# Kernel optimization log

Hardware: AMD Instinct MI355X
Metric: run time of the kernel (lower is better)

The kernel has to match this reference:

```python
import jax, jax.numpy as jnp
import numpy as np

EMB = 1024
HEADS = 16
HEAD_DIM = EMB // HEADS
DFF = 4 * EMB
EPS = 1e-5


def gelu_tanh(x):
    c = jnp.sqrt(jnp.asarray(2.0 / jnp.pi, dtype=x.dtype))
    return 0.5 * x * (1.0 + jnp.tanh(c * (x + 0.044715 * x ** 3)))


def layernorm(x, scale, shift):
    mean = jnp.mean(x, axis=-1, keepdims=True)
    var = jnp.mean((x - mean) ** 2, axis=-1, keepdims=True)
    return scale * ((x - mean) / jnp.sqrt(var + EPS)) + shift


def setup_inputs() -> dict:
    key = jax.random.key(0)
    ks = jax.random.split(key, 12)
    s = 0.02
    return {
        "x": jax.random.normal(ks[0], (2, 2048, EMB), dtype=jnp.float32),
        "Wq": jax.random.normal(ks[1], (EMB, EMB), dtype=jnp.float32) * s,
        "Wk": jax.random.normal(ks[2], (EMB, EMB), dtype=jnp.float32) * s,
        "Wv": jax.random.normal(ks[3], (EMB, EMB), dtype=jnp.float32) * s,
        "Wo": jax.random.normal(ks[4], (EMB, EMB), dtype=jnp.float32) * s,
        "bo": jnp.zeros((EMB,), dtype=jnp.float32),
        "W1": jax.random.normal(ks[5], (EMB, DFF), dtype=jnp.float32) * s,
        "b1": jnp.zeros((DFF,), dtype=jnp.float32),
        "W2": jax.random.normal(ks[6], (DFF, EMB), dtype=jnp.float32) * s,
        "b2": jnp.zeros((EMB,), dtype=jnp.float32),
        "g1": jnp.ones((EMB,), dtype=jnp.float32),
        "s1": jnp.zeros((EMB,), dtype=jnp.float32),
        "g2": jnp.ones((EMB,), dtype=jnp.float32),
        "s2": jnp.zeros((EMB,), dtype=jnp.float32),
    }


def reference(x, Wq, Wk, Wv, Wo, bo, W1, b1, W2, b2, g1, s1, g2, s2):
    B, S, E = x.shape
    # attention sub-block (pre-norm, residual)
    h = layernorm(x, g1, s1)
    Q = (h @ Wq).reshape(B, S, HEADS, HEAD_DIM)
    K = (h @ Wk).reshape(B, S, HEADS, HEAD_DIM)
    V = (h @ Wv).reshape(B, S, HEADS, HEAD_DIM)
    # scores: [B, H, S, S]
    scores = jnp.einsum("bqhd,bkhd->bhqk", Q, K)
    causal = jnp.tril(jnp.ones((S, S), dtype=bool))
    scores = jnp.where(causal, scores, -jnp.inf)
    attn = jax.nn.softmax(scores / np.sqrt(HEAD_DIM), axis=-1)
    ctx = jnp.einsum("bhqk,bkhd->bqhd", attn, V).reshape(B, S, E)
    x = x + (ctx @ Wo + bo)
    # FFN sub-block
    h = layernorm(x, g2, s2)
    h = gelu_tanh(h @ W1 + b1) @ W2 + b2
    return x + h
```

## Files before the change

### kernel.cpp

```cpp
#include <hip/hip_runtime.h>
#include <hip/hip_bf16.h>

typedef __attribute__((ext_vector_type(8))) short short8;
typedef __attribute__((ext_vector_type(4))) float f32x4;

#define EMB   1024
#define DFF   4096
#define S_LEN 2048
#define NB    2
#define MTOT  (NB * S_LEN)
#define HEADS 16
#define HDIM  64
#define QKVN  3072
#define BK    32

__device__ __forceinline__ float bf2f(unsigned short u) {
  return __uint_as_float(((unsigned int)u) << 16);
}
__device__ __forceinline__ unsigned short f2bf(float f) {
  unsigned int x = __float_as_uint(f);
  unsigned int r = (x + 0x7fffu + ((x >> 16) & 1u)) >> 16;
  return (unsigned short)r;
}
__device__ __forceinline__ unsigned int cvtpk(float a, float b) {
  unsigned int r;
  asm("v_cvt_pk_bf16_f32 %0, %1, %2" : "=v"(r) : "v"(a), "v"(b));
  return r;
}

__device__ __forceinline__ void gl_lds16(const unsigned short* g, unsigned short* l) {
  __builtin_amdgcn_global_load_lds(
      (const __attribute__((address_space(1))) unsigned int*)g,
      (__attribute__((address_space(3))) unsigned int*)l, 16, 0, 0);
}

__global__ __launch_bounds__(256) void transpose_to_bf16(
    const float* __restrict__ W, unsigned short* __restrict__ Wt, int K, int N)
{
  __shared__ float t[32][33];
  const int n0 = blockIdx.x * 32, k0 = blockIdx.y * 32;
  const int tx = threadIdx.x, ty = threadIdx.y;
#pragma unroll
  for (int i = 0; i < 4; ++i) {
    int r = ty + i * 8;
    t[r][tx] = W[(size_t)(k0 + r) * N + n0 + tx];
  }
  __syncthreads();
#pragma unroll
  for (int i = 0; i < 4; ++i) {
    int r = ty + i * 8;
    Wt[(size_t)(n0 + r) * K + k0 + tx] = f2bf(t[tx][r]);
  }
}

__global__ __launch_bounds__(256) void transpose_v(
    const unsigned short* __restrict__ qkv, unsigned short* __restrict__ Vt)
{
  __shared__ unsigned short t[32][33];
  const int s0 = blockIdx.x * 32, d0 = blockIdx.y * 32, bh = blockIdx.z;
  const int b = bh >> 4, h = bh & 15;
  const int tx = threadIdx.x, ty = threadIdx.y;
#pragma unroll
  for (int i = 0; i < 4; ++i) {
    int r = ty + i * 8;
    t[r][tx] = qkv[((size_t)(b * S_LEN + s0 + r)) * QKVN + 2048 + h * HDIM + d0 + tx];
  }
  __syncthreads();
#pragma unroll
  for (int i = 0; i < 4; ++i) {
    int r = ty + i * 8;
    Vt[((size_t)bh * HDIM + d0 + r) * S_LEN + s0 + tx] = t[tx][r];
  }
}

__global__ __launch_bounds__(256) void ln_kernel(
    const float* __restrict__ X, const float* __restrict__ g,
    const float* __restrict__ sh, unsigned short* __restrict__ H)
{
  const int row = blockIdx.x, t = threadIdx.x;
  const float* xr = X + (size_t)row * EMB;
  float4 v = *(const float4*)(xr + t * 4);
  float s  = v.x + v.y + v.z + v.w;
  float ss = v.x * v.x + v.y * v.y + v.z * v.z + v.w * v.w;
#pragma unroll
  for (int off = 32; off > 0; off >>= 1) {
    s  += __shfl_xor(s, off);
    ss += __shfl_xor(ss, off);
  }
  __shared__ float rs[4], rss[4];
  const int wid = t >> 6;
  if ((t & 63) == 0) { rs[wid] = s; rss[wid] = ss; }
  __syncthreads();
  s  = rs[0] + rs[1] + rs[2] + rs[3];
  ss = rss[0] + rss[1] + rss[2] + rss[3];
  const float mean = s * (1.f / EMB);
  const float var  = ss * (1.f / EMB) - mean * mean;
  const float rstd = rsqrtf(var + 1e-5f);
  float4 gv = *(const float4*)(g + t * 4);
  float4 sv = *(const float4*)(sh + t * 4);
  ushort4 o;
  o.x = f2bf((v.x - mean) * rstd * gv.x + sv.x);
  o.y = f2bf((v.y - mean) * rstd * gv.y + sv.y);
  o.z = f2bf((v.z - mean) * rstd * gv.z + sv.z);
  o.w = f2bf((v.w - mean) * rstd * gv.w + sv.w);
  *(ushort4*)(H + (size_t)row * EMB + t * 4) = o;
}

__device__ __forceinline__ float gelu_tanh_f(float v) {
  float u = v + 0.044715f * v * v * v;
  float t = tanhf(0.7978845608028654f * u);
  return 0.5f * v * (1.0f + t);
}

template <int MODE, int BN>
__global__ __launch_bounds__(256, 2) void gemm_gl(
    const unsigned short* __restrict__ A, const unsigned short* __restrict__ Bt,
    int M, int N, int Kloop, int Kld,
    const float* __restrict__ bias, const float* __restrict__ resf,
    float* __restrict__ outf, unsigned short* __restrict__ outb)
{
  constexpr int NFRAG = BN / 32;
  __shared__ unsigned short As[2][128 * BK];
  __shared__ unsigned short Bs[2][BN * BK];

  const int tid = threadIdx.x;
  const int lane = tid & 63, wid = tid >> 6;
  const int m0 = blockIdx.y * 128, n0 = blockIdx.x * BN;
  const int wr = wid >> 1, wc = wid & 1;
  const int l16 = lane & 15, kg = lane >> 4;

  const int sr  = lane >> 2;
  const int scs = (((lane & 3) ^ ((lane >> 3) & 3))) * 8;
  const int xr = (l16 >> 1) & 3;

  const unsigned short* Abase = A + (size_t)m0 * Kld;
  const unsigned short* Bbase = Bt + (size_t)n0 * Kld;

  f32x4 acc[4][NFRAG];
#pragma unroll
  for (int i = 0; i < 4; ++i)
#pragma unroll
    for (int j = 0; j < NFRAG; ++j) acc[i][j] = (f32x4){0.f, 0.f, 0.f, 0.f};

  const int nt = Kloop / BK;

#define STAGE(buf, t)                                                          \
  do {                                                                         \
    const int k0_ = (t) * BK;                                                  \
    _Pragma("unroll")                                                          \
    for (int i_ = 0; i_ < 2; ++i_) {                                           \
      const int chunk_ = wid * 2 + i_;                                         \
      gl_lds16(Abase + (size_t)(chunk_ * 16 + sr) * Kld + k0_ + scs,           \
               &As[buf][0] + chunk_ * 512);                                    \
    }                                                                          \
    _Pragma("unroll")                                                          \
    for (int i_ = 0; i_ < BN / 64; ++i_) {                                     \
      const int chunk_ = wid * (BN / 64) + i_;                                 \
      gl_lds16(Bbase + (size_t)(chunk_ * 16 + sr) * Kld + k0_ + scs,           \
               &Bs[buf][0] + chunk_ * 512);                                    \
    }                                                                          \
  } while (0)

  STAGE(0, 0);
  __syncthreads();
  int cur = 0;
  for (int t = 0; t < nt; ++t) {
    if (t + 1 < nt) STAGE(cur ^ 1, t + 1);
    short8 af[4], bfr[NFRAG];
#pragma unroll
    for (int i = 0; i < 4; ++i)
      af[i] = *(const short8*)(&As[cur][(wr * 64 + i * 16 + l16) * BK + (kg ^ xr) * 8]);
#pragma unroll
    for (int j = 0; j < NFRAG; ++j)
      bfr[j] = *(const short8*)(&Bs[cur][(wc * (BN / 2) + j * 16 + l16) * BK + (kg ^ xr) * 8]);
#pragma unroll
    for (int i = 0; i < 4; ++i)
#pragma unroll
      for (int j = 0; j < NFRAG; ++j)
        acc[i][j] = __builtin_amdgcn_mfma_f32_16x16x32_bf16(af[i], bfr[j], acc[i][j], 0, 0, 0);
    __syncthreads();
    cur ^= 1;
  }
#undef STAGE

#pragma unroll
  for (int i = 0; i < 4; ++i) {
#pragma unroll
    for (int j = 0; j < NFRAG; ++j) {
      const int c = n0 + wc * (BN / 2) + j * 16 + l16;
#pragma unroll
      for (int r = 0; r < 4; ++r) {
        const int row = m0 + wr * 64 + i * 16 + kg * 4 + r;
        const size_t idx = (size_t)row * N + c;
        float v = acc[i][j][r];
        if constexpr (MODE == 0) {
          outb[idx] = f2bf(c < 1024 ? v * 0.18033688011112042f : v);
        } else if constexpr (MODE == 1) {
          outf[idx] = v + bias[c] + resf[idx];
        } else if constexpr (MODE == 2) {
          outb[idx] = f2bf(gelu_tanh_f(v + bias[c]));
        } else if constexpr (MODE == 3) {
          outf[idx] = v + bias[c] + resf[idx];
        } else if constexpr (MODE == 4) {
          outb[idx] = f2bf(v);
        } else {
          outf[idx] = v + bias[c] + resf[idx] + bf2f(outb[idx]);
        }
      }
    }
  }
}

__global__ __launch_bounds__(256) void attn_mfma(
    const unsigned short* __restrict__ qkv, const unsigned short* __restrict__ Vt,
    unsigned short* __restrict__ ctx)
{
  __shared__ unsigned short Ks[64][64];
  __shared__ unsigned short Vs[64][64];
  __shared__ unsigned short Ps[4][2][16][64];

  const int tid  = threadIdx.x;
  const int lane = tid & 63, wv = tid >> 6;
  const int l16  = lane & 15, kg = lane >> 4;
  const int bh   = blockIdx.y;
  const int b    = bh >> 4, h = bh & 15;
  const int qtg0 = (int)blockIdx.x;
  const int qtg1 = 31 - (int)blockIdx.x;

  const size_t qbase  = ((size_t)b * S_LEN) * QKVN + h * HDIM;
  const size_t kbase  = qbase + 1024;
  const size_t vtbase = ((size_t)bh * HDIM) * S_LEN;
  const size_t cbase  = ((size_t)b * S_LEN) * EMB + h * HDIM;

  short8 qf[2][2];
#pragma unroll
  for (int g = 0; g < 2; ++g) {
    const int qt = g ? qtg1 : qtg0;
    const unsigned short* qrow =
        qkv + qbase + (size_t)(qt * 64 + wv * 16 + l16) * QKVN;
    qf[g][0] = *(const short8*)(qrow + kg * 8);
    qf[g][1] = *(const short8*)(qrow + 32 + kg * 8);
  }

  f32x4 o[2][4];
#pragma unroll
  for (int g = 0; g < 2; ++g)
#pragma unroll
    for (int dt = 0; dt < 4; ++dt) o[g][dt] = (f32x4){0.f, 0.f, 0.f, 0.f};
  float m[2] = {-1e30f, -1e30f}, l[2] = {0.f, 0.f};

  const int srow = tid >> 2;
  const int c0   = tid & 3;
  const int sx   = srow & 7;
  const int col0 = ((2 * c0)     ^ sx) * 8;
  const int col1 = ((2 * c0 + 1) ^ sx) * 8;
  const int rx   = l16 & 7;
  const int ntiles = qtg1 + 1;

  const unsigned short* ksrc = qkv + kbase + (size_t)srow * QKVN + c0 * 16;
  const unsigned short* vsrc = Vt + vtbase + (size_t)srow * S_LEN + c0 * 16;
  short8 k0 = *(const short8*)(ksrc);
  short8 k1 = *(const short8*)(ksrc + 8);
  short8 v0 = *(const short8*)(vsrc);
  short8 v1 = *(const short8*)(vsrc + 8);

  for (int kt = 0; kt < ntiles; ++kt) {
    __syncthreads();
    *(short8*)(&Ks[srow][col0]) = k0;
    *(short8*)(&Ks[srow][col1]) = k1;
    *(short8*)(&Vs[srow][col0]) = v0;
    *(short8*)(&Vs[srow][col1]) = v1;
    __syncthreads();

    if (kt + 1 < ntiles) {
      const unsigned short* kn =
          qkv + kbase + (size_t)((kt + 1) * 64 + srow) * QKVN + c0 * 16;
      const unsigned short* vn =
          Vt + vtbase + (size_t)srow * S_LEN + (kt + 1) * 64 + c0 * 16;
      k0 = *(const short8*)(kn);
      k1 = *(const short8*)(kn + 8);
      v0 = *(const short8*)(vn);
      v1 = *(const short8*)(vn + 8);
    }

    const bool act0 = (kt <= qtg0);

    short8 kf0[4], kf1[4];
#pragma unroll
    for (int j = 0; j < 4; ++j) {
      kf0[j] = *(const short8*)(&Ks[j * 16 + l16][(kg ^ rx) * 8]);
      kf1[j] = *(const short8*)(&Ks[j * 16 + l16][((kg + 4) ^ rx) * 8]);
    }

    float fac[2] = {1.f, 1.f};
#pragma unroll
    for (int g = 0; g < 2; ++g) {
      if (g == 0 && !act0) continue;
      const int qt = g ? qtg1 : qtg0;

      f32x4 sa[4];
#pragma unroll
      for (int j = 0; j < 4; ++j) {
        sa[j] = (f32x4){0.f, 0.f, 0.f, 0.f};
        sa[j] = __builtin_amdgcn_mfma_f32_16x16x32_bf16(kf0[j], qf[g][0], sa[j], 0, 0, 0);
        sa[j] = __builtin_amdgcn_mfma_f32_16x16x32_bf16(kf1[j], qf[g][1], sa[j], 0, 0, 0);
      }

      if (kt == qt) {
        const int qloc = wv * 16 + l16;
#pragma unroll
        for (int j = 0; j < 4; ++j)
#pragma unroll
          for (int r = 0; r < 4; ++r)
            if (j * 16 + kg * 4 + r > qloc) sa[j][r] = -1e30f;
      }

      float m0j = fmaxf(fmaxf(sa[0][0], sa[0][1]), fmaxf(sa[0][2], sa[0][3]));
      float m1j = fmaxf(fmaxf(sa[1][0], sa[1][1]), fmaxf(sa[1][2], sa[1][3]));
      float m2j = fmaxf(fmaxf(sa[2][0], sa[2][1]), fmaxf(sa[2][2], sa[2][3]));
      float m3j = fmaxf(fmaxf(sa[3][0], sa[3][1]), fmaxf(sa[3][2], sa[3][3]));
      float mx = fmaxf(fmaxf(m0j, m1j), fmaxf(m2j, m3j));
      mx = fmaxf(mx, __shfl_xor(mx, 16));
      mx = fmaxf(mx, __shfl_xor(mx, 32));
      const float mn = fmaxf(m[g], mx);
      fac[g] = exp2f(m[g] - mn);
      m[g] = mn;
      float ps = 0.f;
#pragma unroll
      for (int j = 0; j < 4; ++j) {
        float p0 = exp2f(sa[j][0] - mn);
        float p1 = exp2f(sa[j][1] - mn);
        float p2 = exp2f(sa[j][2] - mn);
        float p3 = exp2f(sa[j][3] - mn);
        sa[j][0] = p0; sa[j][1] = p1; sa[j][2] = p2; sa[j][3] = p3;
        ps += (p0 + p1) + (p2 + p3);
      }
      ps += __shfl_xor(ps, 16);
      ps += __shfl_xor(ps, 32);
      l[g] = l[g] * fac[g] + ps;

#pragma unroll
      for (int j = 0; j < 4; ++j) {
        uint2 pw;
        pw.x = cvtpk(sa[j][0], sa[j][1]);
        pw.y = cvtpk(sa[j][2], sa[j][3]);
        *(uint2*)(&Ps[wv][g][l16][((2 * j + (kg >> 1)) ^ rx) * 8 + (kg & 1) * 4]) = pw;
      }
    }

#pragma unroll
    for (int g = 0; g < 2; ++g) {
      if (g == 0 && !act0) continue;
#pragma unroll
      for (int dt = 0; dt < 4; ++dt)
#pragma unroll
        for (int r = 0; r < 4; ++r) o[g][dt][r] *= fac[g];
    }

    short8 pf[2][2];
#pragma unroll
    for (int g = 0; g < 2; ++g) {
      if (g == 0 && !act0) continue;
      pf[g][0] = *(const short8*)(&Ps[wv][g][l16][(kg ^ rx) * 8]);
      pf[g][1] = *(const short8*)(&Ps[wv][g][l16][((kg + 4) ^ rx) * 8]);
    }
#pragma unroll
    for (int dt = 0; dt < 4; ++dt) {
      short8 vf0 = *(const short8*)(&Vs[dt * 16 + l16][(kg ^ rx) * 8]);
      short8 vf1 = *(const short8*)(&Vs[dt * 16 + l16][((kg + 4) ^ rx) * 8]);
#pragma unroll
      for (int g = 0; g < 2; ++g) {
        if (g == 0 && !act0) continue;
        o[g][dt] = __builtin_amdgcn_mfma_f32_16x16x32_bf16(vf0, pf[g][0], o[g][dt], 0, 0, 0);
        o[g][dt] = __builtin_amdgcn_mfma_f32_16x16x32_bf16(vf1, pf[g][1], o[g][dt], 0, 0, 0);
      }
    }
  }

#pragma unroll
  for (int g = 0; g < 2; ++g) {
    const int qt = g ? qtg1 : qtg0;
    const float inv = 1.0f / l[g];
    const int qrow = qt * 64 + wv * 16 + l16;
#pragma unroll
    for (int dt = 0; dt < 4; ++dt) {
      uint2 cw;
      cw.x = cvtpk(o[g][dt][0] * inv, o[g][dt][1] * inv);
      cw.y = cvtpk(o[g][dt][2] * inv, o[g][dt][3] * inv);
      *(uint2*)(&ctx[cbase + (size_t)qrow * EMB + dt * 16 + kg * 4]) = cw;
    }
  }
}

extern "C" void kernel_launch(void* const* d_in, const int* in_sizes, int n_in,
                              void* d_out, int out_size, void* d_ws, size_t ws_size,
                              hipStream_t stream)
{
  const float* x  = (const float*)d_in[0];
  const float* Wq = (const float*)d_in[1];
  const float* Wk = (const float*)d_in[2];
  const float* Wv = (const float*)d_in[3];
  const float* Wo = (const float*)d_in[4];
  const float* bo = (const float*)d_in[5];
  const float* W1 = (const float*)d_in[6];
  const float* b1 = (const float*)d_in[7];
  const float* W2 = (const float*)d_in[8];
  const float* b2 = (const float*)d_in[9];
  const float* g1 = (const float*)d_in[10];
  const float* s1 = (const float*)d_in[11];
  const float* g2 = (const float*)d_in[12];
  const float* s2 = (const float*)d_in[13];

  float* out = (float*)d_out;
  char* ws = (char*)d_ws;
  const size_t MB = 1024 * 1024;
  unsigned short* wtQ  = (unsigned short*)(ws + 0 * MB);
  unsigned short* wtK  = (unsigned short*)(ws + 2 * MB);
  unsigned short* wtV  = (unsigned short*)(ws + 4 * MB);
  unsigned short* wtO  = (unsigned short*)(ws + 6 * MB);
  unsigned short* wtW1 = (unsigned short*)(ws + 8 * MB);
  unsigned short* wtW2 = (unsigned short*)(ws + 16 * MB);
  unsigned short* h    = (unsigned short*)(ws + 24 * MB);
  unsigned short* qkv  = (unsigned short*)(ws + 32 * MB);
  unsigned short* Vt   = (unsigned short*)(ws + 56 * MB);
  unsigned short* ctxb = h;
  unsigned short* h2   = h;
  unsigned short* pbuf = h;
  unsigned short* gbuf = qkv;

  dim3 tb(32, 8);
  transpose_to_bf16<<<dim3(32, 32),  tb, 0, stream>>>(Wq, wtQ, 1024, 1024);
  transpose_to_bf16<<<dim3(32, 32),  tb, 0, stream>>>(Wk, wtK, 1024, 1024);
  transpose_to_bf16<<<dim3(32, 32),  tb, 0, stream>>>(Wv, wtV, 1024, 1024);
  transpose_to_bf16<<<dim3(32, 32),  tb, 0, stream>>>(Wo, wtO, 1024, 1024);
  transpose_to_bf16<<<dim3(128, 32), tb, 0, stream>>>(W1, wtW1, 1024, 4096);
  transpose_to_bf16<<<dim3(32, 128), tb, 0, stream>>>(W2, wtW2, 4096, 1024);

  ln_kernel<<<MTOT, 256, 0, stream>>>(x, g1, s1, h);

  gemm_gl<0, 128><<<dim3(24, 32), 256, 0, stream>>>(
      h, wtQ, MTOT, QKVN, 1024, 1024, nullptr, nullptr, nullptr, qkv);

  transpose_v<<<dim3(64, 2, 32), tb, 0, stream>>>(qkv, Vt);

  attn_mfma<<<dim3(16, 32), 256, 0, stream>>>(qkv, Vt, ctxb);

  gemm_gl<1, 64><<<dim3(16, 32), 256, 0, stream>>>(
      ctxb, wtO, MTOT, 1024, 1024, 1024, bo, x, out, nullptr);

  ln_kernel<<<MTOT, 256, 0, stream>>>(out, g2, s2, h2);

  gemm_gl<2, 128><<<dim3(32, 32), 256, 0, stream>>>(
      h2, wtW1, MTOT, DFF, 1024, 1024, b1, nullptr, nullptr, gbuf);

  gemm_gl<4, 64><<<dim3(16, 32), 256, 0, stream>>>(
      gbuf + 2048, wtW2 + 2048, MTOT, 1024, 2048, DFF, nullptr, nullptr, nullptr, pbuf);
  gemm_gl<5, 64><<<dim3(16, 32), 256, 0, stream>>>(
      gbuf, wtW2, MTOT, 1024, 2048, DFF, b2, out, out, pbuf);
}
```

Baseline: 287.4 us.

## Fuse weight transposes, XCD-swizzle GEMM/attention grids, add lazy softmax rescale and setprio

```diff
diff --git a/kernel.cpp b/kernel.cpp
--- a/kernel.cpp
+++ b/kernel.cpp
@@ -34,11 +34,28 @@
       (__attribute__((address_space(3))) unsigned int*)l, 16, 0, 0);
 }
 
-__global__ __launch_bounds__(256) void transpose_to_bf16(
-    const float* __restrict__ W, unsigned short* __restrict__ Wt, int K, int N)
+__global__ __launch_bounds__(256) void fused_transpose(
+    const float* __restrict__ Wq, const float* __restrict__ Wk,
+    const float* __restrict__ Wv, const float* __restrict__ Wo,
+    const float* __restrict__ W1, const float* __restrict__ W2,
+    unsigned short* __restrict__ wtQ, unsigned short* __restrict__ wtK,
+    unsigned short* __restrict__ wtV, unsigned short* __restrict__ wtO,
+    unsigned short* __restrict__ wtW1, unsigned short* __restrict__ wtW2)
 {
   __shared__ float t[32][33];
-  const int n0 = blockIdx.x * 32, k0 = blockIdx.y * 32;
+  const int bid = (int)blockIdx.x;
+  const float* W; unsigned short* Wt; int K, N, local;
+  if (bid < 4096) {
+    const int sel = bid >> 10; local = bid & 1023; K = 1024; N = 1024;
+    W  = sel == 0 ? Wq  : sel == 1 ? Wk  : sel == 2 ? Wv  : Wo;
+    Wt = sel == 0 ? wtQ : sel == 1 ? wtK : sel == 2 ? wtV : wtO;
+  } else if (bid < 8192) {
+    local = bid - 4096; K = 1024; N = 4096; W = W1; Wt = wtW1;
+  } else {
+    local = bid - 8192; K = 4096; N = 1024; W = W2; Wt = wtW2;
+  }
+  const int nbx = N >> 5;
+  const int n0 = (local % nbx) * 32, k0 = (local / nbx) * 32;
   const int tx = threadIdx.x, ty = threadIdx.y;
 #pragma unroll
   for (int i = 0; i < 4; ++i) {
@@ -115,7 +132,7 @@
 template <int MODE, int BN>
 __global__ __launch_bounds__(256, 2) void gemm_gl(
     const unsigned short* __restrict__ A, const unsigned short* __restrict__ Bt,
-    int M, int N, int Kloop, int Kld,
+    int M, int N, int Kloop, int Kld, int nbx,
     const float* __restrict__ bias, const float* __restrict__ resf,
     float* __restrict__ outf, unsigned short* __restrict__ outb)
 {
@@ -125,7 +142,13 @@
 
   const int tid = threadIdx.x;
   const int lane = tid & 63, wid = tid >> 6;
-  const int m0 = blockIdx.y * 128, n0 = blockIdx.x * BN;
+  const int nwg = (int)gridDim.x;
+  const int cpx = nwg >> 3;
+  const int bid = (int)blockIdx.x;
+  const int swz = (bid & 7) * cpx + (bid >> 3);
+  const int by = swz / nbx;
+  const int bx = swz - by * nbx;
+  const int m0 = by * 128, n0 = bx * BN;
   const int wr = wid >> 1, wc = wid & 1;
   const int l16 = lane & 15, kg = lane >> 4;
 
@@ -199,8 +222,6 @@
           outf[idx] = v + bias[c] + resf[idx];
         } else if constexpr (MODE == 2) {
           outb[idx] = f2bf(gelu_tanh_f(v + bias[c]));
-        } else if constexpr (MODE == 3) {
-          outf[idx] = v + bias[c] + resf[idx];
         } else if constexpr (MODE == 4) {
           outb[idx] = f2bf(v);
         } else {
@@ -222,10 +243,13 @@
   const int tid  = threadIdx.x;
   const int lane = tid & 63, wv = tid >> 6;
   const int l16  = lane & 15, kg = lane >> 4;
-  const int bh   = blockIdx.y;
+  const int bid  = (int)blockIdx.x;
+  const int swz  = (bid & 7) * 64 + (bid >> 3);
+  const int pair = swz & 15;
+  const int bh   = swz >> 4;
   const int b    = bh >> 4, h = bh & 15;
-  const int qtg0 = (int)blockIdx.x;
-  const int qtg1 = 31 - (int)blockIdx.x;
+  const int qtg0 = pair;
+  const int qtg1 = 31 - pair;
 
   const size_t qbase  = ((size_t)b * S_LEN) * QKVN + h * HDIM;
   const size_t kbase  = qbase + 1024;
@@ -293,18 +317,21 @@
     }
 
     float fac[2] = {1.f, 1.f};
+    bool resc[2] = {false, false};
 #pragma unroll
     for (int g = 0; g < 2; ++g) {
       if (g == 0 && !act0) continue;
       const int qt = g ? qtg1 : qtg0;
 
       f32x4 sa[4];
+      __builtin_amdgcn_s_setprio(1);
 #pragma unroll
       for (int j = 0; j < 4; ++j) {
         sa[j] = (f32x4){0.f, 0.f, 0.f, 0.f};
         sa[j] = __builtin_amdgcn_mfma_f32_16x16x32_bf16(kf0[j], qf[g][0], sa[j], 0, 0, 0);
         sa[j] = __builtin_amdgcn_mfma_f32_16x16x32_bf16(kf1[j], qf[g][1], sa[j], 0, 0, 0);
       }
+      __builtin_amdgcn_s_setprio(0);
 
       if (kt == qt) {
         const int qloc = wv * 16 + l16;
@@ -322,16 +349,20 @@
       float mx = fmaxf(fmaxf(m0j, m1j), fmaxf(m2j, m3j));
       mx = fmaxf(mx, __shfl_xor(mx, 16));
       mx = fmaxf(mx, __shfl_xor(mx, 32));
-      const float mn = fmaxf(m[g], mx);
-      fac[g] = exp2f(m[g] - mn);
-      m[g] = mn;
+      if (!__all(mx - m[g] <= 8.0f)) {
+        const float mn = fmaxf(m[g], mx);
+        fac[g] = exp2f(m[g] - mn);
+        m[g] = mn;
+        resc[g] = true;
+      }
+      const float mcur = m[g];
       float ps = 0.f;
 #pragma unroll
       for (int j = 0; j < 4; ++j) {
-        float p0 = exp2f(sa[j][0] - mn);
-        float p1 = exp2f(sa[j][1] - mn);
-        float p2 = exp2f(sa[j][2] - mn);
-        float p3 = exp2f(sa[j][3] - mn);
+        float p0 = exp2f(sa[j][0] - mcur);
+        float p1 = exp2f(sa[j][1] - mcur);
+        float p2 = exp2f(sa[j][2] - mcur);
+        float p3 = exp2f(sa[j][3] - mcur);
         sa[j][0] = p0; sa[j][1] = p1; sa[j][2] = p2; sa[j][3] = p3;
         ps += (p0 + p1) + (p2 + p3);
       }
@@ -350,11 +381,12 @@
 
 #pragma unroll
     for (int g = 0; g < 2; ++g) {
-      if (g == 0 && !act0) continue;
-#pragma unroll
-      for (int dt = 0; dt < 4; ++dt)
-#pragma unroll
-        for (int r = 0; r < 4; ++r) o[g][dt][r] *= fac[g];
+      if (resc[g]) {
+#pragma unroll
+        for (int dt = 0; dt < 4; ++dt)
+#pragma unroll
+          for (int r = 0; r < 4; ++r) o[g][dt][r] *= fac[g];
+      }
     }
 
     short8 pf[2][2];
@@ -364,6 +396,7 @@
       pf[g][0] = *(const short8*)(&Ps[wv][g][l16][(kg ^ rx) * 8]);
       pf[g][1] = *(const short8*)(&Ps[wv][g][l16][((kg + 4) ^ rx) * 8]);
     }
+    __builtin_amdgcn_s_setprio(1);
 #pragma unroll
     for (int dt = 0; dt < 4; ++dt) {
       short8 vf0 = *(const short8*)(&Vs[dt * 16 + l16][(kg ^ rx) * 8]);
@@ -375,6 +408,7 @@
         o[g][dt] = __builtin_amdgcn_mfma_f32_16x16x32_bf16(vf1, pf[g][1], o[g][dt], 0, 0, 0);
       }
     }
+    __builtin_amdgcn_s_setprio(0);
   }
 
 #pragma unroll
@@ -428,33 +462,28 @@
   unsigned short* pbuf = h;
   unsigned short* gbuf = qkv;
 
-  dim3 tb(32, 8);
-  transpose_to_bf16<<<dim3(32, 32),  tb, 0, stream>>>(Wq, wtQ, 1024, 1024);
-  transpose_to_bf16<<<dim3(32, 32),  tb, 0, stream>>>(Wk, wtK, 1024, 1024);
-  transpose_to_bf16<<<dim3(32, 32),  tb, 0, stream>>>(Wv, wtV, 1024, 1024);
-  transpose_to_bf16<<<dim3(32, 32),  tb, 0, stream>>>(Wo, wtO, 1024, 1024);
-  transpose_to_bf16<<<dim3(128, 32), tb, 0, stream>>>(W1, wtW1, 1024, 4096);
-  transpose_to_bf16<<<dim3(32, 128), tb, 0, stream>>>(W2, wtW2, 4096, 1024);
+  fused_transpose<<<dim3(12288), dim3(32, 8), 0, stream>>>(
+      Wq, Wk, Wv, Wo, W1, W2, wtQ, wtK, wtV, wtO, wtW1, wtW2);
 
   ln_kernel<<<MTOT, 256, 0, stream>>>(x, g1, s1, h);
 
-  gemm_gl<0, 128><<<dim3(24, 32), 256, 0, stream>>>(
-      h, wtQ, MTOT, QKVN, 1024, 1024, nullptr, nullptr, nullptr, qkv);
-
-  transpose_v<<<dim3(64, 2, 32), tb, 0, stream>>>(qkv, Vt);
-
-  attn_mfma<<<dim3(16, 32), 256, 0, stream>>>(qkv, Vt, ctxb);
-
-  gemm_gl<1, 64><<<dim3(16, 32), 256, 0, stream>>>(
-      ctxb, wtO, MTOT, 1024, 1024, 1024, bo, x, out, nullptr);
+  gemm_gl<0, 128><<<dim3(24 * 32), 256, 0, stream>>>(
+      h, wtQ, MTOT, QKVN, 1024, 1024, 24, nullptr, nullptr, nullptr, qkv);
+
+  transpose_v<<<dim3(64, 2, 32), dim3(32, 8), 0, stream>>>(qkv, Vt);
+
+  attn_mfma<<<dim3(512), 256, 0, stream>>>(qkv, Vt, ctxb);
+
+  gemm_gl<1, 64><<<dim3(16 * 32), 256, 0, stream>>>(
+      ctxb, wtO, MTOT, 1024, 1024, 1024, 16, bo, x, out, nullptr);
 
   ln_kernel<<<MTOT, 256, 0, stream>>>(out, g2, s2, h2);
 
-  gemm_gl<2, 128><<<dim3(32, 32), 256, 0, stream>>>(
-      h2, wtW1, MTOT, DFF, 1024, 1024, b1, nullptr, nullptr, gbuf);
-
-  gemm_gl<4, 64><<<dim3(16, 32), 256, 0, stream>>>(
-      gbuf + 2048, wtW2 + 2048, MTOT, 1024, 2048, DFF, nullptr, nullptr, nullptr, pbuf);
-  gemm_gl<5, 64><<<dim3(16, 32), 256, 0, stream>>>(
-      gbuf, wtW2, MTOT, 1024, 2048, DFF, b2, out, out, pbuf);
-}
+  gemm_gl<2, 128><<<dim3(32 * 32), 256, 0, stream>>>(
+      h2, wtW1, MTOT, DFF, 1024, 1024, 32, b1, nullptr, nullptr, gbuf);
+
+  gemm_gl<4, 64><<<dim3(16 * 32), 256, 0, stream>>>(
+      gbuf + 2048, wtW2 + 2048, MTOT, 1024, 2048, DFF, 16, nullptr, nullptr, nullptr, pbuf);
+  gemm_gl<5, 64><<<dim3(16 * 32), 256, 0, stream>>>(
+      gbuf, wtW2, MTOT, 1024, 2048, DFF, 16, b2, out, out, pbuf);
+}
```

Result: faster. 265.1 us (-7.7%).
